# Performance work log

Hardware: AMD Instinct MI355X
Metric: run time of the kernel (lower is better)

The kernel has to match this reference:

```python
import jax, jax.numpy as jnp
import numpy as np

WIN = (8, 7, 7)
SHIFT = (4, 3, 3)
HEADS = 4
DIM = 128
VOL = WIN[0] * WIN[1] * WIN[2]  # 392


def _rel_index():
    coords = np.stack(np.meshgrid(np.arange(WIN[0]), np.arange(WIN[1]), np.arange(WIN[2]), indexing='ij'))
    cf = coords.reshape(3, -1)
    rel = (cf[:, :, None] - cf[:, None, :]).transpose(1, 2, 0).astype(np.int64)
    rel[..., 0] += WIN[0] - 1
    rel[..., 1] += WIN[1] - 1
    rel[..., 2] += WIN[2] - 1
    rel[..., 0] *= (2 * WIN[1] - 1) * (2 * WIN[2] - 1)
    rel[..., 1] *= 2 * WIN[2] - 1
    return rel.sum(-1)  # [VOL, VOL]


def _attn_mask(tp, hp, wp):
    m = np.zeros((tp, hp, wp))
    slices = [((0, -WIN[i]), (-WIN[i], -SHIFT[i]), (-SHIFT[i], None)) for i in range(3)]
    cnt = 0
    for d in slices[0]:
        for h in slices[1]:
            for w in slices[2]:
                m[d[0]:d[1], h[0]:h[1], w[0]:w[1]] = cnt
                cnt += 1
    m = m.reshape(tp // WIN[0], WIN[0], hp // WIN[1], WIN[1], wp // WIN[2], WIN[2])
    m = m.transpose(0, 2, 4, 1, 3, 5).reshape(-1, VOL)  # [nW, VOL]
    diff = m[:, None, :] - m[:, :, None]
    return np.where(diff != 0, -100.0, 0.0).astype(np.float32)  # [nW, VOL, VOL]


_REL_IDX = _rel_index()


def setup_inputs() -> dict:
    key = jax.random.key(0)
    ks = jax.random.split(key, 6)
    return {
        'x': jax.random.normal(ks[0], (2, 16, 56, 56, DIM), dtype=jnp.float32),
        'qkv_weight': jax.random.normal(ks[1], (3 * DIM, DIM), dtype=jnp.float32) * 0.02,
        'qkv_bias': jax.random.normal(ks[2], (3 * DIM,), dtype=jnp.float32) * 0.02,
        'proj_weight': jax.random.normal(ks[3], (DIM, DIM), dtype=jnp.float32) * 0.02,
        'proj_bias': jax.random.normal(ks[4], (DIM,), dtype=jnp.float32) * 0.02,
        'rel_bias_table': jax.random.normal(ks[5], ((2 * WIN[0] - 1) * (2 * WIN[1] - 1) * (2 * WIN[2] - 1), HEADS), dtype=jnp.float32) * 0.02,
    }


def reference(x, qkv_weight, qkv_bias, proj_weight, proj_bias, rel_bias_table):
    b, t, h, w, c = x.shape
    hd = c // HEADS
    nt, nh, nw = t // WIN[0], h // WIN[1], w // WIN[2]
    NW = nt * nh * nw

    # relative position bias: [1, HEADS, VOL, VOL]
    bias = rel_bias_table[jnp.asarray(_REL_IDX.flatten())]
    bias = bias.reshape(VOL, VOL, HEADS).transpose(2, 0, 1)[None]

    # cyclic shift
    xs = jnp.roll(x, shift=(-SHIFT[0], -SHIFT[1], -SHIFT[2]), axis=(1, 2, 3))

    # window partition -> [B*NW, VOL, C]
    xw = xs.reshape(b, nt, WIN[0], nh, WIN[1], nw, WIN[2], c)
    xw = xw.transpose(0, 1, 3, 5, 2, 4, 6, 7).reshape(b * NW, VOL, c)

    qkv = xw @ qkv_weight.T + qkv_bias
    qkv = qkv.reshape(b * NW, VOL, 3, HEADS, hd).transpose(2, 0, 3, 1, 4)
    q, k, v = qkv[0] * (hd ** -0.5), qkv[1], qkv[2]

    attn = jnp.einsum('nhqd,nhkd->nhqk', q, k) + bias
    mask = jnp.asarray(_attn_mask(t, h, w))  # [NW, VOL, VOL]
    attn = attn.reshape(b, NW, HEADS, VOL, VOL) + mask[None, :, None]
    attn = jax.nn.softmax(attn, axis=-1).reshape(b * NW, HEADS, VOL, VOL)

    out = jnp.einsum('nhqk,nhkd->nqhd', attn, v).reshape(b * NW, VOL, c)
    out = out @ proj_weight.T + proj_bias

    # window reverse
    out = out.reshape(b, nt, nh, nw, WIN[0], WIN[1], WIN[2], c)
    out = out.transpose(0, 1, 4, 2, 5, 3, 6, 7).reshape(b, t, h, w, c)
    out = jnp.roll(out, shift=SHIFT, axis=(1, 2, 3))
    return out
```

## Files before the change

### kernel.cpp

```cpp
#include <hip/hip_runtime.h>


#define DIMC   128
#define HEADS  4
#define HD     32
#define VOL    392
#define VPAD   416
#define TQ     400
#define TK     416
#define SCALE2 0.25503490443f
#define LOG2E  1.4426950408889634f
#define MASK2  144.26950408889634f

typedef __bf16 bf16;
typedef __attribute__((ext_vector_type(8))) __bf16 bf16x8;
typedef __attribute__((ext_vector_type(4))) __bf16 bf16x4;
typedef __attribute__((ext_vector_type(4))) float  f32x4;

#define OFF_VT  (392*32)
#define VTCOLS  416
#define LDS_ELEMS (392*32 + 32*VTCOLS)
#define SMEM_A  (LDS_ELEMS*2)
#define AW_BYTES (256ull * VPAD * DIMC * 2ull)

static __device__ inline bf16x8 pack8(float4 a, float4 b) {
    bf16x8 r;
    r[0] = (bf16)a.x; r[1] = (bf16)a.y; r[2] = (bf16)a.z; r[3] = (bf16)a.w;
    r[4] = (bf16)b.x; r[5] = (bf16)b.y; r[6] = (bf16)b.z; r[7] = (bf16)b.w;
    return r;
}
static __device__ inline bf16x8 zero8() {
    bf16x8 z;
#pragma unroll
    for (int i = 0; i < 8; ++i) z[i] = (bf16)0.0f;
    return z;
}
static __device__ inline int swz4(int row) { return ((row >> 1) ^ (row >> 3)) & 3; }

static __device__ inline unsigned pkbf(float a, float b) {
    unsigned short ua = __builtin_bit_cast(unsigned short, (bf16)a);
    unsigned short ub = __builtin_bit_cast(unsigned short, (bf16)b);
    return (unsigned)ua | ((unsigned)ub << 16);
}

#if defined(__has_builtin)
#if __has_builtin(__builtin_amdgcn_exp2f)
#define HAS_EXP2 1
#endif
#endif
static __device__ inline float exp2_hw(float x) {
#ifdef HAS_EXP2
    return __builtin_amdgcn_exp2f(x);
#else
    float r; asm volatile("v_exp_f32 %0, %1\n\ts_nop 0" : "=v"(r) : "v"(x)); return r;
#endif
}

__global__ __launch_bounds__(256) void gen_table(const float* __restrict__ btab,
                                                 bf16* __restrict__ tbl) {
    const int idx = blockIdx.x * 256 + threadIdx.x;
    const int total = 8 * HEADS * TQ * (TK / 4);
    if (idx >= total) return;
    const int k4  = (idx % (TK / 4)) * 4;
    const int q   = (idx / (TK / 4)) % TQ;
    const int h   = (idx / ((TK / 4) * TQ)) & 3;
    const int pat = idx / ((TK / 4) * TQ * HEADS);
    const int tb = (pat >> 2) & 1, hb = (pat >> 1) & 1, wb = pat & 1;

    int qt = 0, qh = 0, qw = 0, lq = 0;
    if (q < VOL) {
        qt = q / 49; const int qr = q - qt * 49; qh = qr / 7; qw = qr - qh * 7;
        lq = (tb ? (qt < 4 ? 1 : 2) : 0) * 9 + (hb ? (qh < 4 ? 1 : 2) : 0) * 3 +
             (wb ? (qw < 4 ? 1 : 2) : 0);
    }
    bf16x4 out;
#pragma unroll
    for (int j = 0; j < 4; ++j) {
        const int k = k4 + j;
        float v;
        if (k >= VOL)      v = -30000.0f;
        else if (q >= VOL) v = 0.0f;
        else {
            const int kt = k / 49; const int kr = k - kt * 49;
            const int kh = kr / 7; const int kw = kr - kh * 7;
            const int rel = ((qt - kt + 7) * 13 + (qh - kh + 6)) * 13 + (qw - kw + 6);
            v = btab[rel * HEADS + h] * LOG2E;
            const int lk = (tb ? (kt < 4 ? 1 : 2) : 0) * 9 +
                           (hb ? (kh < 4 ? 1 : 2) : 0) * 3 +
                           (wb ? (kw < 4 ? 1 : 2) : 0);
            if (lq != lk) v -= MASK2;
        }
        out[j] = (bf16)v;
    }
    *(bf16x4*)&tbl[((size_t)(pat * HEADS + h) * TQ + q) * TK + k4] = out;
}

#define NJ 7

__global__ __attribute__((amdgpu_flat_work_group_size(256, 256),
                          amdgpu_waves_per_eu(2, 4)))
void swin_attn(
    const float* __restrict__ x, const float* __restrict__ wqkv,
    const float* __restrict__ bqkv, const bf16* __restrict__ tbl,
    bf16* __restrict__ aw)
{
    const int bid  = blockIdx.x;
    const int xcd  = bid & 7;
    const int tt   = bid >> 3;
    const int win  = xcd * 32 + (tt >> 2);
    const int head = tt & 3;
    const int b    = win >> 7;
    const int wrem = win & 127;
    const int it   = wrem >> 6;
    const int ih   = (wrem >> 3) & 7;
    const int iw   = wrem & 7;
    const int pat  = ((it == 1) ? 4 : 0) | ((ih == 7) ? 2 : 0) | ((iw == 7) ? 1 : 0);

    const int tid  = threadIdx.x;
    const int lane = tid & 63;
    const int wv   = tid >> 6;
    const int l16  = lane & 15;
    const int lg   = lane >> 4;

    extern __shared__ char smem[];
    bf16* lds = (bf16*)smem;
    const bf16* tblh = tbl + (size_t)(pat * HEADS + head) * (TQ * TK);

    bf16x8 wfr[6][4];
    float  bcol[4];
#pragma unroll
    for (int o = 0; o < 6; ++o) {
        const int g = o >> 1, h2 = o & 1;
        const int wrow = g * DIMC + head * HD + h2 * 16 + l16;
        const float* wp = wqkv + (size_t)wrow * DIMC + 8 * lg;
#pragma unroll
        for (int ks = 0; ks < 4; ++ks)
            wfr[o][ks] = pack8(*(const float4*)(wp + ks * 32),
                               *(const float4*)(wp + ks * 32 + 4));
        if (o < 4) bcol[o] = bqkv[wrow];
    }
    float bvr[2][4];
#pragma unroll
    for (int h2 = 0; h2 < 2; ++h2)
#pragma unroll
        for (int r = 0; r < 4; ++r)
            bvr[h2][r] = bqkv[2 * DIMC + head * HD + h2 * 16 + lg * 4 + r];

    bf16x8 qf[NJ];
#pragma unroll
    for (int j = 0; j < NJ; ++j) qf[j] = zero8();

#pragma unroll
    for (int j = 0; j < NJ; ++j) {
        const int mt = wv + 4 * j;
        if (mt < 26) {
            const int tv = mt * 16 + l16;
            bf16x8 af[4];
            if (tv < VOL) {
                const int lt = tv / 49, rr = tv - lt * 49;
                const int lh = rr / 7,  lw = rr - lh * 7;
                const int t0 = (it * 8 + lt + 4) & 15;
                int h0 = ih * 7 + lh + 3; if (h0 >= 56) h0 -= 56;
                int w0 = iw * 7 + lw + 3; if (w0 >= 56) w0 -= 56;
                const float* xp = x + (size_t)(((b * 16 + t0) * 56 + h0) * 56 + w0) * DIMC + 8 * lg;
#pragma unroll
                for (int ks = 0; ks < 4; ++ks)
                    af[ks] = pack8(*(const float4*)(xp + ks * 32),
                                   *(const float4*)(xp + ks * 32 + 4));
            } else {
#pragma unroll
                for (int ks = 0; ks < 4; ++ks) af[ks] = zero8();
            }
#pragma unroll
            for (int o = 0; o < 2; ++o) {
                f32x4 acc = {0.f, 0.f, 0.f, 0.f};
#pragma unroll
                for (int ks = 0; ks < 4; ++ks)
                    acc = __builtin_amdgcn_mfma_f32_16x16x32_bf16(af[ks], wfr[o][ks], acc, 0, 0, 0);
                const int cb = (o & 1) * 16 + l16;
#pragma unroll
                for (int r = 0; r < 4; ++r) {
                    const int row = mt * 16 + lg * 4 + r;
                    if (row < VOL)
                        lds[row * 32 + (cb ^ (swz4(row) << 3))] = (bf16)((acc[r] + bcol[o]) * SCALE2);
                }
            }
            if (mt < 25) {
                const int qr = (tv < VOL) ? tv : (VOL - 1);
                qf[j] = *(const bf16x8*)&lds[qr * 32 + ((lg * 8) ^ (swz4(qr) << 3))];
            }
#pragma unroll
            for (int o = 2; o < 4; ++o) {
                f32x4 acc = {0.f, 0.f, 0.f, 0.f};
#pragma unroll
                for (int ks = 0; ks < 4; ++ks)
                    acc = __builtin_amdgcn_mfma_f32_16x16x32_bf16(af[ks], wfr[o][ks], acc, 0, 0, 0);
                const int cb = (o & 1) * 16 + l16;
#pragma unroll
                for (int r = 0; r < 4; ++r) {
                    const int row = mt * 16 + lg * 4 + r;
                    if (row < VOL)
                        lds[row * 32 + (cb ^ (swz4(row) << 3))] = (bf16)(acc[r] + bcol[o]);
                }
            }
#pragma unroll
            for (int h2 = 0; h2 < 2; ++h2) {
                f32x4 acc = {0.f, 0.f, 0.f, 0.f};
#pragma unroll
                for (int ks = 0; ks < 4; ++ks)
                    acc = __builtin_amdgcn_mfma_f32_16x16x32_bf16(wfr[4 + h2][ks], af[ks], acc, 0, 0, 0);
#pragma unroll
                for (int r = 0; r < 4; ++r) {
                    const int n = h2 * 16 + lg * 4 + r;
                    lds[OFF_VT + n * VTCOLS + (tv ^ (swz4(n) << 3))] = (bf16)(acc[r] + bvr[h2][r]);
                }
            }
        }
    }
    __syncthreads();

    {
        const int c = l16 & 3, d = l16 >> 2;
        const int rowA  = c + 8 * d;
        const int swzA  = (c >> 1) ^ d;
        const int swzB  = (2 + (c >> 1)) ^ d;
        const int kbA   = rowA * 32       + ((lg * 8) ^ (swzA << 3));
        const int kbB   = (rowA + 4) * 32 + ((lg * 8) ^ (swzB << 3));
        const int vb0   = OFF_VT + l16 * VTCOLS        + ((lg * 8) ^ (swz4(l16) << 3));
        const int vb1   = OFF_VT + (16 + l16) * VTCOLS + ((lg * 8) ^ (swz4(16 + l16) << 3));

        int    tbOff[NJ];
        f32x4  o0[NJ], o1[NJ];
        float  sum[NJ];
#pragma unroll
        for (int j = 0; j < NJ; ++j) {
            const int qtok = (wv + 4 * j) * 16 + l16;
            const int qc   = (qtok < TQ) ? qtok : (TQ - 1);
            tbOff[j] = (qc * TK + 8 * lg) * 2;
            o0[j] = f32x4{0.f, 0.f, 0.f, 0.f};
            o1[j] = f32x4{0.f, 0.f, 0.f, 0.f};
            sum[j] = 0.f;
        }

        uint4 bufA[NJ], bufB[NJ];
#pragma unroll
        for (int j = 0; j < NJ; ++j)
            bufA[j] = *(const uint4*)((const char*)tblh + tbOff[j]);

#define CH_BODY(CH, CUR)                                                      \
        {                                                                     \
            const int ch = (CH);                                              \
            const bf16x8 kfA = *(const bf16x8*)&lds[kbA + ch * 1024];         \
            const bf16x8 kfB = *(const bf16x8*)&lds[kbB + ch * 1024];         \
            const bf16x8 v0  = *(const bf16x8*)&lds[vb0 + ch * 32];           \
            const bf16x8 v1  = *(const bf16x8*)&lds[vb1 + ch * 32];           \
            _Pragma("unroll")                                                 \
            for (int j = 0; j < NJ; ++j) {                                    \
                if (wv + 4 * j < 25) {                                        \
                    const uint4 bu = CUR[j];                                  \
                    f32x4 cA, cB;                                             \
                    cA[0] = __builtin_bit_cast(float, bu.x << 16);            \
                    cA[1] = __builtin_bit_cast(float, bu.x & 0xffff0000u);    \
                    cA[2] = __builtin_bit_cast(float, bu.y << 16);            \
                    cA[3] = __builtin_bit_cast(float, bu.y & 0xffff0000u);    \
                    cB[0] = __builtin_bit_cast(float, bu.z << 16);            \
                    cB[1] = __builtin_bit_cast(float, bu.z & 0xffff0000u);    \
                    cB[2] = __builtin_bit_cast(float, bu.w << 16);            \
                    cB[3] = __builtin_bit_cast(float, bu.w & 0xffff0000u);    \
                    const f32x4 sA = __builtin_amdgcn_mfma_f32_16x16x32_bf16(kfA, qf[j], cA, 0, 0, 0); \
                    const f32x4 sB = __builtin_amdgcn_mfma_f32_16x16x32_bf16(kfB, qf[j], cB, 0, 0, 0); \
                    float pA[4], pB[4];                                       \
                    _Pragma("unroll")                                         \
                    for (int r = 0; r < 4; ++r) {                             \
                        pA[r] = exp2_hw(sA[r]);                               \
                        pB[r] = exp2_hw(sB[r]);                               \
                        sum[j] += pA[r] + pB[r];                              \
                    }                                                         \
                    union { unsigned u[4]; bf16x8 v; } pw;                    \
                    pw.u[0] = pkbf(pA[0], pA[1]); pw.u[1] = pkbf(pA[2], pA[3]); \
                    pw.u[2] = pkbf(pB[0], pB[1]); pw.u[3] = pkbf(pB[2], pB[3]); \
                    o0[j] = __builtin_amdgcn_mfma_f32_16x16x32_bf16(v0, pw.v, o0[j], 0, 0, 0); \
                    o1[j] = __builtin_amdgcn_mfma_f32_16x16x32_bf16(v1, pw.v, o1[j], 0, 0, 0); \
                }                                                             \
            }                                                                 \
        }
#define CH_PRE(CH, DST)                                                       \
        {                                                                     \
            const int chp_ = (CH) < 12 ? (CH) : 12;                           \
            _Pragma("unroll")                                                 \
            for (int j = 0; j < NJ; ++j)                                      \
                DST[j] = *(const uint4*)((const char*)tblh + tbOff[j] + chp_ * 64); \
        }

#pragma unroll 1
        for (int chp = 0; chp < 12; chp += 2) {
            CH_PRE(chp + 1, bufB)
            CH_BODY(chp, bufA)
            CH_PRE(chp + 2, bufA)
            CH_BODY(chp + 1, bufB)
        }
        CH_BODY(12, bufA)
#undef CH_BODY
#undef CH_PRE

#pragma unroll
        for (int j = 0; j < NJ; ++j) {
            const int mt   = wv + 4 * j;
            const int qtok = mt * 16 + l16;
            if (mt < 25) {
                float s = sum[j];
                s += __shfl_xor(s, 16);
                s += __shfl_xor(s, 32);
                const float inv = 1.0f / s;
                if (qtok < VOL) {
                    bf16x4 w0, w1;
#pragma unroll
                    for (int r = 0; r < 4; ++r) {
                        w0[r] = (bf16)(o0[j][r] * inv);
                        w1[r] = (bf16)(o1[j][r] * inv);
                    }
                    bf16* op = aw + ((size_t)win * VPAD + qtok) * DIMC + head * HD + lg * 4;
                    *(bf16x4*)op = w0;
                    *(bf16x4*)(op + 16) = w1;
                }
            }
        }
    }
}

__global__ __launch_bounds__(256, 2) void swin_proj(
    const bf16* __restrict__ aw, const float* __restrict__ wproj,
    const float* __restrict__ bproj, float* __restrict__ out)
{
    const int bid  = blockIdx.x;
    const int xcd  = bid & 7;
    const int rest = bid >> 3;
    const int win  = xcd * 32 + (rest & 31);
    const int half = rest >> 5;
    const int b    = win >> 7;
    const int wrem = win & 127;
    const int it   = wrem >> 6;
    const int ih   = (wrem >> 3) & 7;
    const int iw   = wrem & 7;

    const int tid  = threadIdx.x;
    const int lane = tid & 63;
    const int wid  = tid >> 6;
    const int l16  = lane & 15;
    const int lg   = lane >> 4;

    const int mt_end = half ? 25 : 13;
    for (int mt = 13 * half + wid; mt < mt_end; mt += 4) {
        bf16x8 af[4];
        const bf16* ap = aw + ((size_t)win * VPAD + mt * 16 + l16) * DIMC + 8 * lg;
#pragma unroll
        for (int ks = 0; ks < 4; ++ks) af[ks] = *(const bf16x8*)(ap + ks * 32);

        float* ob[4]; bool qok[4];
#pragma unroll
        for (int r = 0; r < 4; ++r) {
            int q = mt * 16 + lg * 4 + r;
            qok[r] = q < VOL; if (!qok[r]) q = 0;
            const int lt = q / 49, rr = q - lt * 49;
            const int lh = rr / 7, lw = rr - lh * 7;
            const int t0 = (it * 8 + lt + 4) & 15;
            int h0 = ih * 7 + lh + 3; if (h0 >= 56) h0 -= 56;
            int w0 = iw * 7 + lw + 3; if (w0 >= 56) w0 -= 56;
            ob[r] = out + (size_t)(((b * 16 + t0) * 56 + h0) * 56 + w0) * DIMC;
        }
#pragma unroll
        for (int nt = 0; nt < 8; ++nt) {
            f32x4 acc = {0.f, 0.f, 0.f, 0.f};
            const float* wp = wproj + (size_t)(nt * 16 + l16) * DIMC + 8 * lg;
#pragma unroll
            for (int ks = 0; ks < 4; ++ks) {
                float4 u0 = *(const float4*)(wp + ks * 32);
                float4 u1 = *(const float4*)(wp + ks * 32 + 4);
                acc = __builtin_amdgcn_mfma_f32_16x16x32_bf16(af[ks], pack8(u0, u1), acc, 0, 0, 0);
            }
            const float bv = bproj[nt * 16 + l16];
#pragma unroll
            for (int r = 0; r < 4; ++r)
                if (qok[r]) ob[r][nt * 16 + l16] = acc[r] + bv;
        }
    }
}

extern "C" void kernel_launch(void* const* d_in, const int* in_sizes, int n_in,
                              void* d_out, int out_size, void* d_ws, size_t ws_size,
                              hipStream_t stream) {
    const float* x     = (const float*)d_in[0];
    const float* wqkv  = (const float*)d_in[1];
    const float* bqkv  = (const float*)d_in[2];
    const float* wproj = (const float*)d_in[3];
    const float* bproj = (const float*)d_in[4];
    const float* btab  = (const float*)d_in[5];
    bf16*  aw  = (bf16*)d_ws;
    bf16*  tbl = (bf16*)((char*)d_ws + AW_BYTES);
    float* out = (float*)d_out;

    const int tbl_threads = 8 * HEADS * TQ * (TK / 4);
    gen_table<<<dim3((tbl_threads + 255) / 256), dim3(256), 0, stream>>>(btab, tbl);
    swin_attn<<<dim3(1024), dim3(256), SMEM_A, stream>>>(x, wqkv, bqkv, tbl, aw);
    swin_proj<<<dim3(512), dim3(256), 0, stream>>>(aw, wproj, bproj, out);
}
```

Baseline: 134.3 us.

## Double attention block to 512 threads and split QK/V projection phases

Result: slower. 170.9 us (+27.2%).

```diff
diff --git a/kernel.cpp b/kernel.cpp
--- a/kernel.cpp
+++ b/kernel.cpp
@@ -95,9 +95,9 @@
     *(bf16x4*)&tbl[((size_t)(pat * HEADS + h) * TQ + q) * TK + k4] = out;
 }
 
-#define NJ 7
-
-__global__ __attribute__((amdgpu_flat_work_group_size(256, 256),
+#define NJ 4
+
+__global__ __attribute__((amdgpu_flat_work_group_size(512, 512),
                           amdgpu_waves_per_eu(2, 4)))
 void swin_attn(
     const float* __restrict__ x, const float* __restrict__ wqkv,
@@ -126,97 +126,130 @@
     bf16* lds = (bf16*)smem;
     const bf16* tblh = tbl + (size_t)(pat * HEADS + head) * (TQ * TK);
 
-    bf16x8 wfr[6][4];
-    float  bcol[4];
-#pragma unroll
-    for (int o = 0; o < 6; ++o) {
-        const int g = o >> 1, h2 = o & 1;
-        const int wrow = g * DIMC + head * HD + h2 * 16 + l16;
-        const float* wp = wqkv + (size_t)wrow * DIMC + 8 * lg;
-#pragma unroll
-        for (int ks = 0; ks < 4; ++ks)
-            wfr[o][ks] = pack8(*(const float4*)(wp + ks * 32),
-                               *(const float4*)(wp + ks * 32 + 4));
-        if (o < 4) bcol[o] = bqkv[wrow];
-    }
-    float bvr[2][4];
-#pragma unroll
-    for (int h2 = 0; h2 < 2; ++h2)
-#pragma unroll
-        for (int r = 0; r < 4; ++r)
-            bvr[h2][r] = bqkv[2 * DIMC + head * HD + h2 * 16 + lg * 4 + r];
-
     bf16x8 qf[NJ];
 #pragma unroll
     for (int j = 0; j < NJ; ++j) qf[j] = zero8();
 
-#pragma unroll
-    for (int j = 0; j < NJ; ++j) {
-        const int mt = wv + 4 * j;
-        if (mt < 26) {
-            const int tv = mt * 16 + l16;
-            bf16x8 af[4];
-            if (tv < VOL) {
-                const int lt = tv / 49, rr = tv - lt * 49;
-                const int lh = rr / 7,  lw = rr - lh * 7;
-                const int t0 = (it * 8 + lt + 4) & 15;
-                int h0 = ih * 7 + lh + 3; if (h0 >= 56) h0 -= 56;
-                int w0 = iw * 7 + lw + 3; if (w0 >= 56) w0 -= 56;
-                const float* xp = x + (size_t)(((b * 16 + t0) * 56 + h0) * 56 + w0) * DIMC + 8 * lg;
-#pragma unroll
-                for (int ks = 0; ks < 4; ++ks)
-                    af[ks] = pack8(*(const float4*)(xp + ks * 32),
-                                   *(const float4*)(xp + ks * 32 + 4));
-            } else {
-#pragma unroll
-                for (int ks = 0; ks < 4; ++ks) af[ks] = zero8();
+#define X_PTR(tv)                                                             \
+    ({ const int lt_ = (tv) / 49, rr_ = (tv) - lt_ * 49;                      \
+       const int lh_ = rr_ / 7, lw_ = rr_ - lh_ * 7;                          \
+       const int t0_ = (it * 8 + lt_ + 4) & 15;                               \
+       int h0_ = ih * 7 + lh_ + 3; if (h0_ >= 56) h0_ -= 56;                  \
+       int w0_ = iw * 7 + lw_ + 3; if (w0_ >= 56) w0_ -= 56;                  \
+       x + (size_t)(((b * 16 + t0_) * 56 + h0_) * 56 + w0_) * DIMC + 8 * lg; })
+
+    {
+        bf16x8 wqk[4][4];
+        float  bcol[4];
+#pragma unroll
+        for (int o = 0; o < 4; ++o) {
+            const int wrow = (o >> 1) * DIMC + head * HD + (o & 1) * 16 + l16;
+            const float* wp = wqkv + (size_t)wrow * DIMC + 8 * lg;
+#pragma unroll
+            for (int ks = 0; ks < 4; ++ks)
+                wqk[o][ks] = pack8(*(const float4*)(wp + ks * 32),
+                                   *(const float4*)(wp + ks * 32 + 4));
+            bcol[o] = bqkv[wrow];
+        }
+#pragma unroll
+        for (int j = 0; j < NJ; ++j) {
+            const int mt = wv + 8 * j;
+            if (mt < 26) {
+                const int tv = mt * 16 + l16;
+                bf16x8 af[4];
+                if (tv < VOL) {
+                    const float* xp = X_PTR(tv);
+#pragma unroll
+                    for (int ks = 0; ks < 4; ++ks)
+                        af[ks] = pack8(*(const float4*)(xp + ks * 32),
+                                       *(const float4*)(xp + ks * 32 + 4));
+                } else {
+#pragma unroll
+                    for (int ks = 0; ks < 4; ++ks) af[ks] = zero8();
+                }
+#pragma unroll
+                for (int o = 0; o < 2; ++o) {
+                    f32x4 acc = {0.f, 0.f, 0.f, 0.f};
+#pragma unroll
+                    for (int ks = 0; ks < 4; ++ks)
+                        acc = __builtin_amdgcn_mfma_f32_16x16x32_bf16(af[ks], wqk[o][ks], acc, 0, 0, 0);
+                    const int cb = (o & 1) * 16 + l16;
+#pragma unroll
+                    for (int r = 0; r < 4; ++r) {
+                        const int row = mt * 16 + lg * 4 + r;
+                        if (row < VOL)
+                            lds[row * 32 + (cb ^ (swz4(row) << 3))] = (bf16)((acc[r] + bcol[o]) * SCALE2);
+                    }
+                }
+                if (mt < 25) {
+                    const int qr = (tv < VOL) ? tv : (VOL - 1);
+                    qf[j] = *(const bf16x8*)&lds[qr * 32 + ((lg * 8) ^ (swz4(qr) << 3))];
+                }
+#pragma unroll
+                for (int o = 2; o < 4; ++o) {
+                    f32x4 acc = {0.f, 0.f, 0.f, 0.f};
+#pragma unroll
+                    for (int ks = 0; ks < 4; ++ks)
+                        acc = __builtin_amdgcn_mfma_f32_16x16x32_bf16(af[ks], wqk[o][ks], acc, 0, 0, 0);
+                    const int cb = (o & 1) * 16 + l16;
+#pragma unroll
+                    for (int r = 0; r < 4; ++r) {
+                        const int row = mt * 16 + lg * 4 + r;
+                        if (row < VOL)
+                            lds[row * 32 + (cb ^ (swz4(row) << 3))] = (bf16)(acc[r] + bcol[o]);
+                    }
+                }
             }
-#pragma unroll
-            for (int o = 0; o < 2; ++o) {
-                f32x4 acc = {0.f, 0.f, 0.f, 0.f};
-#pragma unroll
-                for (int ks = 0; ks < 4; ++ks)
-                    acc = __builtin_amdgcn_mfma_f32_16x16x32_bf16(af[ks], wfr[o][ks], acc, 0, 0, 0);
-                const int cb = (o & 1) * 16 + l16;
-#pragma unroll
-                for (int r = 0; r < 4; ++r) {
-                    const int row = mt * 16 + lg * 4 + r;
-                    if (row < VOL)
-                        lds[row * 32 + (cb ^ (swz4(row) << 3))] = (bf16)((acc[r] + bcol[o]) * SCALE2);
+        }
+    }
+
+    {
+        bf16x8 wvv[2][4];
+        float  bvr[2][4];
+#pragma unroll
+        for (int h2 = 0; h2 < 2; ++h2) {
+            const int wrow = 2 * DIMC + head * HD + h2 * 16 + l16;
+            const float* wp = wqkv + (size_t)wrow * DIMC + 8 * lg;
+#pragma unroll
+            for (int ks = 0; ks < 4; ++ks)
+                wvv[h2][ks] = pack8(*(const float4*)(wp + ks * 32),
+                                    *(const float4*)(wp + ks * 32 + 4));
+#pragma unroll
+            for (int r = 0; r < 4; ++r)
+                bvr[h2][r] = bqkv[2 * DIMC + head * HD + h2 * 16 + lg * 4 + r];
+        }
+#pragma unroll
+        for (int j = 0; j < NJ; ++j) {
+            const int mt = wv + 8 * j;
+            if (mt < 26) {
+                const int tv = mt * 16 + l16;
+                bf16x8 af[4];
+                if (tv < VOL) {
+                    const float* xp = X_PTR(tv);
+#pragma unroll
+                    for (int ks = 0; ks < 4; ++ks)
+                        af[ks] = pack8(*(const float4*)(xp + ks * 32),
+                                       *(const float4*)(xp + ks * 32 + 4));
+                } else {
+#pragma unroll
+                    for (int ks = 0; ks < 4; ++ks) af[ks] = zero8();
+                }
+#pragma unroll
+                for (int h2 = 0; h2 < 2; ++h2) {
+                    f32x4 acc = {0.f, 0.f, 0.f, 0.f};
+#pragma unroll
+                    for (int ks = 0; ks < 4; ++ks)
+                        acc = __builtin_amdgcn_mfma_f32_16x16x32_bf16(wvv[h2][ks], af[ks], acc, 0, 0, 0);
+#pragma unroll
+                    for (int r = 0; r < 4; ++r) {
+                        const int n = h2 * 16 + lg * 4 + r;
+                        lds[OFF_VT + n * VTCOLS + (tv ^ (swz4(n) << 3))] = (bf16)(acc[r] + bvr[h2][r]);
+                    }
                 }
             }
-            if (mt < 25) {
-                const int qr = (tv < VOL) ? tv : (VOL - 1);
-                qf[j] = *(const bf16x8*)&lds[qr * 32 + ((lg * 8) ^ (swz4(qr) << 3))];
-            }
-#pragma unroll
-            for (int o = 2; o < 4; ++o) {
-                f32x4 acc = {0.f, 0.f, 0.f, 0.f};
-#pragma unroll
-                for (int ks = 0; ks < 4; ++ks)
-                    acc = __builtin_amdgcn_mfma_f32_16x16x32_bf16(af[ks], wfr[o][ks], acc, 0, 0, 0);
-                const int cb = (o & 1) * 16 + l16;
-#pragma unroll
-                for (int r = 0; r < 4; ++r) {
-                    const int row = mt * 16 + lg * 4 + r;
-                    if (row < VOL)
-                        lds[row * 32 + (cb ^ (swz4(row) << 3))] = (bf16)(acc[r] + bcol[o]);
-                }
-            }
-#pragma unroll
-            for (int h2 = 0; h2 < 2; ++h2) {
-                f32x4 acc = {0.f, 0.f, 0.f, 0.f};
-#pragma unroll
-                for (int ks = 0; ks < 4; ++ks)
-                    acc = __builtin_amdgcn_mfma_f32_16x16x32_bf16(wfr[4 + h2][ks], af[ks], acc, 0, 0, 0);
-#pragma unroll
-                for (int r = 0; r < 4; ++r) {
-                    const int n = h2 * 16 + lg * 4 + r;
-                    lds[OFF_VT + n * VTCOLS + (tv ^ (swz4(n) << 3))] = (bf16)(acc[r] + bvr[h2][r]);
-                }
-            }
-        }
-    }
+        }
+    }
+#undef X_PTR
     __syncthreads();
 
     {
@@ -234,7 +267,7 @@
         float  sum[NJ];
 #pragma unroll
         for (int j = 0; j < NJ; ++j) {
-            const int qtok = (wv + 4 * j) * 16 + l16;
+            const int qtok = (wv + 8 * j) * 16 + l16;
             const int qc   = (qtok < TQ) ? qtok : (TQ - 1);
             tbOff[j] = (qc * TK + 8 * lg) * 2;
             o0[j] = f32x4{0.f, 0.f, 0.f, 0.f};
@@ -256,7 +289,7 @@
             const bf16x8 v1  = *(const bf16x8*)&lds[vb1 + ch * 32];           \
             _Pragma("unroll")                                                 \
             for (int j = 0; j < NJ; ++j) {                                    \
-                if (wv + 4 * j < 25) {                                        \
+                if (wv + 8 * j < 25) {                                        \
                     const uint4 bu = CUR[j];                                  \
                     f32x4 cA, cB;                                             \
                     cA[0] = __builtin_bit_cast(float, bu.x << 16);            \
@@ -305,7 +338,7 @@
 
 #pragma unroll
         for (int j = 0; j < NJ; ++j) {
-            const int mt   = wv + 4 * j;
+            const int mt   = wv + 8 * j;
             const int qtok = mt * 16 + l16;
             if (mt < 25) {
                 float s = sum[j];
@@ -401,6 +434,6 @@
 
     const int tbl_threads = 8 * HEADS * TQ * (TK / 4);
     gen_table<<<dim3((tbl_threads + 255) / 256), dim3(256), 0, stream>>>(btab, tbl);
-    swin_attn<<<dim3(1024), dim3(256), SMEM_A, stream>>>(x, wqkv, bqkv, tbl, aw);
+    swin_attn<<<dim3(1024), dim3(512), SMEM_A, stream>>>(x, wqkv, bqkv, tbl, aw);
     swin_proj<<<dim3(512), dim3(256), 0, stream>>>(aw, wproj, bproj, out);
 }
```
